# Performance work log

Hardware: AMD Instinct MI355X
Metric: run time of the kernel (lower is better)

## Reference

```python
import jax, jax.numpy as jnp
import numpy as np

N_NODES = 100000


def _sage_conv(x, src, dst, w_self, w_neigh, b):
    # DGL SAGEConv('mean'): fc_self(x) + fc_neigh(mean of in-neighbor feats) + bias
    msgs = x[src]                                        # [E, d] gather
    agg = jax.ops.segment_sum(msgs, dst, num_segments=N_NODES)   # [N, d]
    deg = jax.ops.segment_sum(jnp.ones_like(dst, dtype=x.dtype), dst,
                              num_segments=N_NODES)      # [N]
    mean = agg / jnp.maximum(deg, 1.0)[:, None]          # zero-degree -> 0
    return x @ w_self + mean @ w_neigh + b


def setup_inputs() -> dict:
    key = jax.random.key(0)
    ks = jax.random.split(key, 8)
    E, D_IN, D_HID, D_OUT = 1000000, 64, 64, 32
    features = jax.random.normal(ks[0], (N_NODES, D_IN), dtype=jnp.float32)
    src = jax.random.randint(ks[1], (E,), 0, N_NODES, dtype=jnp.int32)
    dst = jax.random.randint(ks[2], (E,), 0, N_NODES, dtype=jnp.int32)
    s = lambda k, i, o: jax.random.normal(k, (i, o), dtype=jnp.float32) / np.sqrt(i)
    return {
        "features": features, "src": src, "dst": dst,
        "w_self1": s(ks[3], D_IN, D_HID), "w_neigh1": s(ks[4], D_IN, D_HID),
        "b1": jnp.zeros((D_HID,), jnp.float32),
        "w_self2": s(ks[5], D_HID, D_OUT), "w_neigh2": s(ks[6], D_HID, D_OUT),
        "b2": jnp.zeros((D_OUT,), jnp.float32),
    }


def reference(features, src, dst, w_self1, w_neigh1, b1, w_self2, w_neigh2, b2):
    h = _sage_conv(features, src, dst, w_self1, w_neigh1, b1)
    h = jax.nn.relu(h)
    # dropout: identity (inference mode)
    h = _sage_conv(h, src, dst, w_self2, w_neigh2, b2)
    return h
```

## Files before the change

kernel.cpp:

```cpp
#include <hip/hip_runtime.h>


#define SPAN        128
#define SPAN_SHIFT  7
#define PART_BLOCK  1024
#define PART_EPT    4
#define NBMAX       1024
#define LDS_S       72

typedef __attribute__((ext_vector_type(8))) short bf16x8;
typedef __attribute__((ext_vector_type(4))) float f32x4;

__device__ __forceinline__ unsigned bf16_rne(float f) {
    unsigned u = __float_as_uint(f);
    return (u + 0x7FFFu + ((u >> 16) & 1u)) >> 16;
}
__device__ __forceinline__ float bf_lo(unsigned u) { return __uint_as_float(u << 16); }
__device__ __forceinline__ float bf_hi(unsigned u) { return __uint_as_float(u & 0xFFFF0000u); }

__global__ __launch_bounds__(PART_BLOCK) void k_partition(
    const int* __restrict__ src, const int* __restrict__ dst,
    int* __restrict__ cursor, unsigned int* __restrict__ pairs,
    int E, int cap,
    const float* __restrict__ feat, unsigned short* __restrict__ xh, long total8,
    const float* __restrict__ ws1, const float* __restrict__ wn1,
    const float* __restrict__ ws2, const float* __restrict__ wn2,
    unsigned short* __restrict__ wt)
{
    const int tid = threadIdx.x;
    for (long i = (long)blockIdx.x * PART_BLOCK + tid; i < total8;
         i += (long)gridDim.x * PART_BLOCK) {
        const float4 a = ((const float4*)feat)[i * 2];
        const float4 b = ((const float4*)feat)[i * 2 + 1];
        uint4 o;
        o.x = bf16_rne(a.x) | (bf16_rne(a.y) << 16);
        o.y = bf16_rne(a.z) | (bf16_rne(a.w) << 16);
        o.z = bf16_rne(b.x) | (bf16_rne(b.y) << 16);
        o.w = bf16_rne(b.z) | (bf16_rne(b.w) << 16);
        ((uint4*)xh)[i] = o;
    }
    if (blockIdx.x < 12) {
        int j = blockIdx.x * PART_BLOCK + tid;
        int mat = j >> 12, rem = j & 4095;
        int c = rem >> 6, k = rem & 63;
        float v;
        if (mat == 0)      v = ws1[k * 64 + c];
        else if (mat == 1) v = wn1[k * 64 + c];
        else               v = (c < 32) ? wn2[k * 32 + c] : ws2[k * 32 + (c - 32)];
        wt[(mat << 12) + (c << 6) + k] = (unsigned short)bf16_rne(v);
    }

    __shared__ int cnt[NBMAX];
    __shared__ int gbase[NBMAX];
    __shared__ int lcur[NBMAX];
    cnt[tid] = 0; lcur[tid] = 0;
    __syncthreads();

    int sv[PART_EPT], bv[PART_EPT];
    const int e0 = blockIdx.x * (PART_BLOCK * PART_EPT) + tid;
    #pragma unroll
    for (int j = 0; j < PART_EPT; ++j) {
        int e = e0 + j * PART_BLOCK;
        bv[j] = -1;
        if (e < E) {
            int s = src[e], d = dst[e];
            bv[j] = d >> SPAN_SHIFT;
            sv[j] = s | ((d & (SPAN - 1)) << 24);
            atomicAdd(&cnt[bv[j]], 1);
        }
    }
    __syncthreads();
    if (cnt[tid] > 0) gbase[tid] = atomicAdd(&cursor[tid], cnt[tid]);
    __syncthreads();
    #pragma unroll
    for (int j = 0; j < PART_EPT; ++j) {
        if (bv[j] >= 0) {
            int r = gbase[bv[j]] + atomicAdd(&lcur[bv[j]], 1);
            if (r < cap) pairs[(size_t)bv[j] * cap + r] = (unsigned int)sv[j];
        }
    }
}

__global__ __launch_bounds__(256) void k_bucket_csr(
    unsigned int* __restrict__ pairs,
    const int* __restrict__ cursor,
    int* __restrict__ starts, int* __restrict__ degs,
    int N, int cap)
{
    __shared__ int cnt[SPAN];
    __shared__ int pref[SPAN];
    __shared__ int lcur[SPAN];
    extern __shared__ unsigned int sorted[];
    const int tid = threadIdx.x;
    const int b = blockIdx.x;
    if (tid < SPAN) { cnt[tid] = 0; lcur[tid] = 0; }
    __syncthreads();

    int m = cursor[b]; if (m > cap) m = cap;
    const size_t pb = (size_t)b * cap;

    for (int i = tid; i < m; i += 256)
        atomicAdd(&cnt[pairs[pb + i] >> 24], 1);
    __syncthreads();

    if (tid < SPAN) pref[tid] = cnt[tid];
    __syncthreads();
    for (int off = 1; off < SPAN; off <<= 1) {
        int v = 0;
        if (tid < SPAN && tid >= off) v = pref[tid - off];
        __syncthreads();
        if (tid < SPAN) pref[tid] += v;
        __syncthreads();
    }

    for (int i = tid; i < m; i += 256) {
        unsigned int p = pairs[pb + i];
        int r = p >> 24;
        int base = (r == 0) ? 0 : pref[r - 1];
        int pos = base + atomicAdd(&lcur[r], 1);
        sorted[pos] = p & 0xFFFFFFu;
    }
    __syncthreads();
    for (int i = tid; i < m; i += 256) pairs[pb + i] = sorted[i];
    if (tid < SPAN) {
        int node = (b << SPAN_SHIFT) + tid;
        if (node < N) {
            int base = (tid == 0) ? 0 : pref[tid - 1];
            starts[node] = (int)pb + base;
            degs[node]   = cnt[tid];
        }
    }
}

__global__ __launch_bounds__(256) void k_gather_b64(
    const unsigned short* __restrict__ xh,
    const unsigned int* __restrict__ esrc,
    const int* __restrict__ starts, const int* __restrict__ degs,
    unsigned short* __restrict__ meanh, int n)
{
    const int w = threadIdx.x >> 6, lane = threadIdx.x & 63;
    const int g = lane >> 4, c = lane & 15;
    const int v0 = (blockIdx.x * 4 + w) * 4;
    if (v0 >= n) return;

    int e[4], end[4], deg[4];
    #pragma unroll
    for (int j = 0; j < 4; ++j) {
        int v = v0 + j;
        if (v < n) { int b = starts[v]; deg[j] = degs[v]; e[j] = b + g; end[j] = b + deg[j]; }
        else { deg[j] = 0; e[j] = 0; end[j] = 0; }
    }
    float acc[4][4];
    #pragma unroll
    for (int j = 0; j < 4; ++j)
        #pragma unroll
        for (int k = 0; k < 4; ++k) acc[j][k] = 0.f;

    while ((e[0] < end[0]) | (e[1] < end[1]) | (e[2] < end[2]) | (e[3] < end[3])) {
        uint2 u[4]; float m[4];
        #pragma unroll
        for (int j = 0; j < 4; ++j) {
            bool p = e[j] < end[j];
            m[j] = p ? 1.f : 0.f;
            int idx = p ? e[j] : 0;
            int s = (int)(esrc[idx] & 0xFFFFFFu);
            s = s < n ? s : n - 1;
            u[j] = *(const uint2*)&xh[(size_t)s * 64 + c * 4];
        }
        #pragma unroll
        for (int j = 0; j < 4; ++j) {
            acc[j][0] = fmaf(m[j], bf_lo(u[j].x), acc[j][0]);
            acc[j][1] = fmaf(m[j], bf_hi(u[j].x), acc[j][1]);
            acc[j][2] = fmaf(m[j], bf_lo(u[j].y), acc[j][2]);
            acc[j][3] = fmaf(m[j], bf_hi(u[j].y), acc[j][3]);
            e[j] += 4;
        }
    }
    #pragma unroll
    for (int j = 0; j < 4; ++j) {
        #pragma unroll
        for (int d = 16; d <= 32; d <<= 1) {
            #pragma unroll
            for (int k = 0; k < 4; ++k) acc[j][k] += __shfl_xor(acc[j][k], d);
        }
        if (lane < 16 && v0 + j < n) {
            float f = deg[j] ? 1.f / (float)deg[j] : 0.f;
            uint2 o;
            o.x = bf16_rne(acc[j][0] * f) | (bf16_rne(acc[j][1] * f) << 16);
            o.y = bf16_rne(acc[j][2] * f) | (bf16_rne(acc[j][3] * f) << 16);
            *(uint2*)&meanh[(size_t)(v0 + j) * 64 + c * 4] = o;
        }
    }
}

__global__ __launch_bounds__(256) void k_gemm_mfma(
    const unsigned short* __restrict__ xh,
    const unsigned short* __restrict__ meanh,
    const unsigned short* __restrict__ wt,
    const float* __restrict__ b1, const float* __restrict__ b2,
    unsigned short* __restrict__ t2,
    float* __restrict__ outp,
    int n)
{
    __shared__ __align__(16) unsigned short sX[128 * LDS_S];
    __shared__ __align__(16) unsigned short sWt[3 * 64 * LDS_S];
    const int tid  = threadIdx.x;
    const int w    = tid >> 6, lane = tid & 63;
    const int quad = lane >> 4, lm = lane & 15;
    const int gm0  = blockIdx.x * 128;
    const int rowA = w * 32;

    for (int i = tid; i < 1536; i += 256) {
        int r  = i >> 3;
        int k0 = (i & 7) << 3;
        *(uint4*)&sWt[r * LDS_S + k0] = *(const uint4*)&wt[(r << 6) + k0];
    }
    for (int i = tid; i < 1024; i += 256) {
        int m = i >> 3, k0 = (i & 7) << 3;
        int gm = gm0 + m;
        uint4 v = make_uint4(0, 0, 0, 0);
        if (gm < n) v = *(const uint4*)&xh[(size_t)gm * 64 + k0];
        *(uint4*)&sX[m * LDS_S + k0] = v;
    }
    __syncthreads();

    f32x4 acc[2][4];
    #pragma unroll
    for (int mt = 0; mt < 2; ++mt)
        #pragma unroll
        for (int nt = 0; nt < 4; ++nt) acc[mt][nt] = (f32x4){0.f, 0.f, 0.f, 0.f};

    #pragma unroll
    for (int kt = 0; kt < 2; ++kt) {
        bf16x8 a0 = *(const bf16x8*)&sX[(rowA + lm) * LDS_S + kt * 32 + quad * 8];
        bf16x8 a1 = *(const bf16x8*)&sX[(rowA + 16 + lm) * LDS_S + kt * 32 + quad * 8];
        #pragma unroll
        for (int nt = 0; nt < 4; ++nt) {
            bf16x8 b = *(const bf16x8*)&sWt[(nt * 16 + lm) * LDS_S + kt * 32 + quad * 8];
            acc[0][nt] = __builtin_amdgcn_mfma_f32_16x16x32_bf16(a0, b, acc[0][nt], 0, 0, 0);
            acc[1][nt] = __builtin_amdgcn_mfma_f32_16x16x32_bf16(a1, b, acc[1][nt], 0, 0, 0);
        }
    }
    __syncthreads();
    for (int i = tid; i < 1024; i += 256) {
        int m = i >> 3, k0 = (i & 7) << 3;
        int gm = gm0 + m;
        uint4 v = make_uint4(0, 0, 0, 0);
        if (gm < n) v = *(const uint4*)&meanh[(size_t)gm * 64 + k0];
        *(uint4*)&sX[m * LDS_S + k0] = v;
    }
    __syncthreads();
    #pragma unroll
    for (int kt = 0; kt < 2; ++kt) {
        bf16x8 a0 = *(const bf16x8*)&sX[(rowA + lm) * LDS_S + kt * 32 + quad * 8];
        bf16x8 a1 = *(const bf16x8*)&sX[(rowA + 16 + lm) * LDS_S + kt * 32 + quad * 8];
        #pragma unroll
        for (int nt = 0; nt < 4; ++nt) {
            bf16x8 b = *(const bf16x8*)&sWt[(64 + nt * 16 + lm) * LDS_S + kt * 32 + quad * 8];
            acc[0][nt] = __builtin_amdgcn_mfma_f32_16x16x32_bf16(a0, b, acc[0][nt], 0, 0, 0);
            acc[1][nt] = __builtin_amdgcn_mfma_f32_16x16x32_bf16(a1, b, acc[1][nt], 0, 0, 0);
        }
    }
    __syncthreads();

    #pragma unroll
    for (int nt = 0; nt < 4; ++nt) {
        float bb = b1[nt * 16 + lm];
        #pragma unroll
        for (int mt = 0; mt < 2; ++mt) {
            int rbase = rowA + mt * 16 + quad * 4;
            #pragma unroll
            for (int r = 0; r < 4; ++r) {
                float hv = fmaxf(acc[mt][nt][r] + bb, 0.f);
                sX[(rbase + r) * LDS_S + nt * 16 + lm] = (unsigned short)bf16_rne(hv);
            }
        }
    }

    f32x4 acc2[2][4];
    #pragma unroll
    for (int mt = 0; mt < 2; ++mt)
        #pragma unroll
        for (int nt = 0; nt < 4; ++nt) acc2[mt][nt] = (f32x4){0.f, 0.f, 0.f, 0.f};
    #pragma unroll
    for (int kt = 0; kt < 2; ++kt) {
        bf16x8 a0 = *(const bf16x8*)&sX[(rowA + lm) * LDS_S + kt * 32 + quad * 8];
        bf16x8 a1 = *(const bf16x8*)&sX[(rowA + 16 + lm) * LDS_S + kt * 32 + quad * 8];
        #pragma unroll
        for (int nt = 0; nt < 4; ++nt) {
            bf16x8 b = *(const bf16x8*)&sWt[(128 + nt * 16 + lm) * LDS_S + kt * 32 + quad * 8];
            acc2[0][nt] = __builtin_amdgcn_mfma_f32_16x16x32_bf16(a0, b, acc2[0][nt], 0, 0, 0);
            acc2[1][nt] = __builtin_amdgcn_mfma_f32_16x16x32_bf16(a1, b, acc2[1][nt], 0, 0, 0);
        }
    }

    #pragma unroll
    for (int mt = 0; mt < 2; ++mt) {
        int rbase = gm0 + rowA + mt * 16 + quad * 4;
        #pragma unroll
        for (int nt = 0; nt < 2; ++nt) {
            #pragma unroll
            for (int r = 0; r < 4; ++r) {
                int gm = rbase + r;
                if (gm < n)
                    t2[(size_t)gm * 32 + nt * 16 + lm] =
                        (unsigned short)bf16_rne(acc2[mt][nt][r]);
            }
        }
        #pragma unroll
        for (int nt = 2; nt < 4; ++nt) {
            float bb = b2[(nt - 2) * 16 + lm];
            #pragma unroll
            for (int r = 0; r < 4; ++r) {
                int gm = rbase + r;
                if (gm < n)
                    outp[(size_t)gm * 32 + (nt - 2) * 16 + lm] = acc2[mt][nt][r] + bb;
            }
        }
    }
}

__global__ __launch_bounds__(256) void k_gather_b32add(
    const unsigned short* __restrict__ t2,
    const unsigned int* __restrict__ esrc,
    const int* __restrict__ starts, const int* __restrict__ degs,
    float* __restrict__ outp, int n)
{
    const int w = threadIdx.x >> 6, lane = threadIdx.x & 63;
    const int g = lane >> 3, c = lane & 7;
    const int v0 = (blockIdx.x * 4 + w) * 4;
    if (v0 >= n) return;

    int e[4], end[4], deg[4];
    #pragma unroll
    for (int j = 0; j < 4; ++j) {
        int v = v0 + j;
        if (v < n) { int b = starts[v]; deg[j] = degs[v]; e[j] = b + g; end[j] = b + deg[j]; }
        else { deg[j] = 0; e[j] = 0; end[j] = 0; }
    }
    float acc[4][4];
    #pragma unroll
    for (int j = 0; j < 4; ++j)
        #pragma unroll
        for (int k = 0; k < 4; ++k) acc[j][k] = 0.f;

    while ((e[0] < end[0]) | (e[1] < end[1]) | (e[2] < end[2]) | (e[3] < end[3])) {
        uint2 u[4]; float m[4];
        #pragma unroll
        for (int j = 0; j < 4; ++j) {
            bool p = e[j] < end[j];
            m[j] = p ? 1.f : 0.f;
            int idx = p ? e[j] : 0;
            int s = (int)(esrc[idx] & 0xFFFFFFu);
            s = s < n ? s : n - 1;
            u[j] = *(const uint2*)&t2[(size_t)s * 32 + c * 4];
        }
        #pragma unroll
        for (int j = 0; j < 4; ++j) {
            acc[j][0] = fmaf(m[j], bf_lo(u[j].x), acc[j][0]);
            acc[j][1] = fmaf(m[j], bf_hi(u[j].x), acc[j][1]);
            acc[j][2] = fmaf(m[j], bf_lo(u[j].y), acc[j][2]);
            acc[j][3] = fmaf(m[j], bf_hi(u[j].y), acc[j][3]);
            e[j] += 8;
        }
    }
    #pragma unroll
    for (int j = 0; j < 4; ++j) {
        #pragma unroll
        for (int d = 8; d <= 32; d <<= 1) {
            #pragma unroll
            for (int k = 0; k < 4; ++k) acc[j][k] += __shfl_xor(acc[j][k], d);
        }
        if (lane < 8 && v0 + j < n && deg[j] > 0) {
            float f = 1.f / (float)deg[j];
            float4 o = *(const float4*)&outp[(size_t)(v0 + j) * 32 + c * 4];
            o.x += acc[j][0] * f; o.y += acc[j][1] * f;
            o.z += acc[j][2] * f; o.w += acc[j][3] * f;
            *(float4*)&outp[(size_t)(v0 + j) * 32 + c * 4] = o;
        }
    }
}

extern "C" void kernel_launch(void* const* d_in, const int* in_sizes, int n_in,
                              void* d_out, int out_size, void* d_ws, size_t ws_size,
                              hipStream_t stream) {
    const float* feat = (const float*)d_in[0];
    const int*   src  = (const int*)d_in[1];
    const int*   dst  = (const int*)d_in[2];
    const float* ws1  = (const float*)d_in[3];
    const float* wn1  = (const float*)d_in[4];
    const float* b1   = (const float*)d_in[5];
    const float* ws2  = (const float*)d_in[6];
    const float* wn2  = (const float*)d_in[7];
    const float* b2   = (const float*)d_in[8];
    float* out = (float*)d_out;

    const int N = in_sizes[0] / 64;
    const int E = in_sizes[1];
    const int nB = (N + SPAN - 1) >> SPAN_SHIFT;

    int cap = ((E + nB - 1) / nB);
    cap = ((cap + cap / 4) + 63) & ~63;
    {
        size_t fixedBytes = NBMAX * 4 + 3 * 4096 * 2 + (size_t)N * 8
                          + (size_t)N * 64 * 2 * 2
                          + (size_t)N * 32 * 2
                          + 16384;
        size_t remain = (ws_size > fixedBytes) ? (ws_size - fixedBytes) : 0;
        size_t capMax = remain / ((size_t)nB * 4);
        if ((size_t)cap > capMax) cap = (int)(capMax & ~(size_t)3);
    }

    char* base = (char*)d_ws;
    int* cursor = (int*)base;
    unsigned short* wt = (unsigned short*)(base + NBMAX * 4);
    unsigned int* pairs = (unsigned int*)(base + NBMAX * 4 + 24576);
    size_t sOff = ((size_t)NBMAX * 4 + 24576 + (size_t)nB * cap * 4 + 4096 + 255) & ~(size_t)255;
    int* starts = (int*)(base + sOff);
    int* degs   = starts + N;
    size_t mOff = (sOff + (size_t)N * 8 + 255) & ~(size_t)255;
    unsigned short* meanh = (unsigned short*)(base + mOff);
    unsigned short* xh    = meanh + (size_t)N * 64;
    unsigned short* t2    = xh + (size_t)N * 64;

    hipMemsetAsync(cursor, 0, NBMAX * 4, stream);

    const long total8 = (long)N * 64 / 8;
    const int pblocks = (E + PART_BLOCK * PART_EPT - 1) / (PART_BLOCK * PART_EPT);
    k_partition<<<pblocks, PART_BLOCK, 0, stream>>>(
        src, dst, cursor, pairs, E, cap,
        feat, xh, total8, ws1, wn1, ws2, wn2, wt);
    k_bucket_csr<<<nB, 256, (size_t)cap * 4, stream>>>(pairs, cursor, starts, degs, N, cap);

    const int gblocks = (N + 15) / 16;
    const int tblocks = (N + 127) / 128;

    k_gather_b64<<<gblocks, 256, 0, stream>>>(xh, pairs, starts, degs, meanh, N);
    k_gemm_mfma<<<tblocks, 256, 0, stream>>>(xh, meanh, wt, b1, b2, t2, out, N);
    k_gather_b32add<<<gblocks, 256, 0, stream>>>(t2, pairs, starts, degs, out, N);
}
```

Before: 181.6 us.

## Fuse layer-1 neighbor mean gather into the MFMA GEMM kernel

```diff
diff --git a/kernel.cpp b/kernel.cpp
--- a/kernel.cpp
+++ b/kernel.cpp
@@ -132,70 +132,10 @@
     }
 }
 
-__global__ __launch_bounds__(256) void k_gather_b64(
+__global__ __launch_bounds__(256) void k_fused(
     const unsigned short* __restrict__ xh,
     const unsigned int* __restrict__ esrc,
     const int* __restrict__ starts, const int* __restrict__ degs,
-    unsigned short* __restrict__ meanh, int n)
-{
-    const int w = threadIdx.x >> 6, lane = threadIdx.x & 63;
-    const int g = lane >> 4, c = lane & 15;
-    const int v0 = (blockIdx.x * 4 + w) * 4;
-    if (v0 >= n) return;
-
-    int e[4], end[4], deg[4];
-    #pragma unroll
-    for (int j = 0; j < 4; ++j) {
-        int v = v0 + j;
-        if (v < n) { int b = starts[v]; deg[j] = degs[v]; e[j] = b + g; end[j] = b + deg[j]; }
-        else { deg[j] = 0; e[j] = 0; end[j] = 0; }
-    }
-    float acc[4][4];
-    #pragma unroll
-    for (int j = 0; j < 4; ++j)
-        #pragma unroll
-        for (int k = 0; k < 4; ++k) acc[j][k] = 0.f;
-
-    while ((e[0] < end[0]) | (e[1] < end[1]) | (e[2] < end[2]) | (e[3] < end[3])) {
-        uint2 u[4]; float m[4];
-        #pragma unroll
-        for (int j = 0; j < 4; ++j) {
-            bool p = e[j] < end[j];
-            m[j] = p ? 1.f : 0.f;
-            int idx = p ? e[j] : 0;
-            int s = (int)(esrc[idx] & 0xFFFFFFu);
-            s = s < n ? s : n - 1;
-            u[j] = *(const uint2*)&xh[(size_t)s * 64 + c * 4];
-        }
-        #pragma unroll
-        for (int j = 0; j < 4; ++j) {
-            acc[j][0] = fmaf(m[j], bf_lo(u[j].x), acc[j][0]);
-            acc[j][1] = fmaf(m[j], bf_hi(u[j].x), acc[j][1]);
-            acc[j][2] = fmaf(m[j], bf_lo(u[j].y), acc[j][2]);
-            acc[j][3] = fmaf(m[j], bf_hi(u[j].y), acc[j][3]);
-            e[j] += 4;
-        }
-    }
-    #pragma unroll
-    for (int j = 0; j < 4; ++j) {
-        #pragma unroll
-        for (int d = 16; d <= 32; d <<= 1) {
-            #pragma unroll
-            for (int k = 0; k < 4; ++k) acc[j][k] += __shfl_xor(acc[j][k], d);
-        }
-        if (lane < 16 && v0 + j < n) {
-            float f = deg[j] ? 1.f / (float)deg[j] : 0.f;
-            uint2 o;
-            o.x = bf16_rne(acc[j][0] * f) | (bf16_rne(acc[j][1] * f) << 16);
-            o.y = bf16_rne(acc[j][2] * f) | (bf16_rne(acc[j][3] * f) << 16);
-            *(uint2*)&meanh[(size_t)(v0 + j) * 64 + c * 4] = o;
-        }
-    }
-}
-
-__global__ __launch_bounds__(256) void k_gemm_mfma(
-    const unsigned short* __restrict__ xh,
-    const unsigned short* __restrict__ meanh,
     const unsigned short* __restrict__ wt,
     const float* __restrict__ b1, const float* __restrict__ b2,
     unsigned short* __restrict__ t2,
@@ -215,8 +155,8 @@
         int k0 = (i & 7) << 3;
         *(uint4*)&sWt[r * LDS_S + k0] = *(const uint4*)&wt[(r << 6) + k0];
     }
-    for (int i = tid; i < 1024; i += 256) {
-        int m = i >> 3, k0 = (i & 7) << 3;
+    for (int i = lane; i < 256; i += 64) {
+        int m = rowA + (i >> 3), k0 = (i & 7) << 3;
         int gm = gm0 + m;
         uint4 v = make_uint4(0, 0, 0, 0);
         if (gm < n) v = *(const uint4*)&xh[(size_t)gm * 64 + k0];
@@ -241,15 +181,59 @@
             acc[1][nt] = __builtin_amdgcn_mfma_f32_16x16x32_bf16(a1, b, acc[1][nt], 0, 0, 0);
         }
     }
-    __syncthreads();
-    for (int i = tid; i < 1024; i += 256) {
-        int m = i >> 3, k0 = (i & 7) << 3;
-        int gm = gm0 + m;
-        uint4 v = make_uint4(0, 0, 0, 0);
-        if (gm < n) v = *(const uint4*)&meanh[(size_t)gm * 64 + k0];
-        *(uint4*)&sX[m * LDS_S + k0] = v;
-    }
-    __syncthreads();
+
+    for (int grp = 0; grp < 8; ++grp) {
+        const int v0 = gm0 + rowA + grp * 4;
+        int e[4], end[4], dg[4];
+        #pragma unroll
+        for (int j = 0; j < 4; ++j) {
+            int v = v0 + j;
+            if (v < n) { int b = starts[v]; dg[j] = degs[v]; e[j] = b + quad; end[j] = b + dg[j]; }
+            else { dg[j] = 0; e[j] = 0; end[j] = 0; }
+        }
+        float ga[4][4];
+        #pragma unroll
+        for (int j = 0; j < 4; ++j)
+            #pragma unroll
+            for (int k = 0; k < 4; ++k) ga[j][k] = 0.f;
+
+        while ((e[0] < end[0]) | (e[1] < end[1]) | (e[2] < end[2]) | (e[3] < end[3])) {
+            uint2 u[4]; float m[4];
+            #pragma unroll
+            for (int j = 0; j < 4; ++j) {
+                bool p = e[j] < end[j];
+                m[j] = p ? 1.f : 0.f;
+                int idx = p ? e[j] : 0;
+                int s = (int)(esrc[idx] & 0xFFFFFFu);
+                s = s < n ? s : n - 1;
+                u[j] = *(const uint2*)&xh[(size_t)s * 64 + lm * 4];
+            }
+            #pragma unroll
+            for (int j = 0; j < 4; ++j) {
+                ga[j][0] = fmaf(m[j], bf_lo(u[j].x), ga[j][0]);
+                ga[j][1] = fmaf(m[j], bf_hi(u[j].x), ga[j][1]);
+                ga[j][2] = fmaf(m[j], bf_lo(u[j].y), ga[j][2]);
+                ga[j][3] = fmaf(m[j], bf_hi(u[j].y), ga[j][3]);
+                e[j] += 4;
+            }
+        }
+        #pragma unroll
+        for (int j = 0; j < 4; ++j) {
+            #pragma unroll
+            for (int d = 16; d <= 32; d <<= 1) {
+                #pragma unroll
+                for (int k = 0; k < 4; ++k) ga[j][k] += __shfl_xor(ga[j][k], d);
+            }
+            if (lane < 16 && v0 + j < n) {
+                float f = dg[j] ? 1.f / (float)dg[j] : 0.f;
+                uint2 o;
+                o.x = bf16_rne(ga[j][0] * f) | (bf16_rne(ga[j][1] * f) << 16);
+                o.y = bf16_rne(ga[j][2] * f) | (bf16_rne(ga[j][3] * f) << 16);
+                *(uint2*)&sX[(rowA + grp * 4 + j) * LDS_S + lm * 4] = o;
+            }
+        }
+    }
+
     #pragma unroll
     for (int kt = 0; kt < 2; ++kt) {
         bf16x8 a0 = *(const bf16x8*)&sX[(rowA + lm) * LDS_S + kt * 32 + quad * 8];
@@ -261,7 +245,6 @@
             acc[1][nt] = __builtin_amdgcn_mfma_f32_16x16x32_bf16(a1, b, acc[1][nt], 0, 0, 0);
         }
     }
-    __syncthreads();
 
     #pragma unroll
     for (int nt = 0; nt < 4; ++nt) {
@@ -403,7 +386,7 @@
     cap = ((cap + cap / 4) + 63) & ~63;
     {
         size_t fixedBytes = NBMAX * 4 + 3 * 4096 * 2 + (size_t)N * 8
-                          + (size_t)N * 64 * 2 * 2
+                          + (size_t)N * 64 * 2
                           + (size_t)N * 32 * 2
                           + 16384;
         size_t remain = (ws_size > fixedBytes) ? (ws_size - fixedBytes) : 0;
@@ -419,9 +402,8 @@
     int* starts = (int*)(base + sOff);
     int* degs   = starts + N;
     size_t mOff = (sOff + (size_t)N * 8 + 255) & ~(size_t)255;
-    unsigned short* meanh = (unsigned short*)(base + mOff);
-    unsigned short* xh    = meanh + (size_t)N * 64;
-    unsigned short* t2    = xh + (size_t)N * 64;
+    unsigned short* xh = (unsigned short*)(base + mOff);
+    unsigned short* t2 = xh + (size_t)N * 64;
 
     hipMemsetAsync(cursor, 0, NBMAX * 4, stream);
 
@@ -435,7 +417,6 @@
     const int gblocks = (N + 15) / 16;
     const int tblocks = (N + 127) / 128;
 
-    k_gather_b64<<<gblocks, 256, 0, stream>>>(xh, pairs, starts, degs, meanh, N);
-    k_gemm_mfma<<<tblocks, 256, 0, stream>>>(xh, meanh, wt, b1, b2, t2, out, N);
+    k_fused<<<tblocks, 256, 0, stream>>>(xh, pairs, starts, degs, wt, b1, b2, t2, out, N);
     k_gather_b32add<<<gblocks, 256, 0, stream>>>(t2, pairs, starts, degs, out, N);
 }
```

Measured after the change: 223.0 us. 22.7% more time.
